# Performance work log

Measured on AMD Instinct MI355X. Metric: run time of the kernel, lower is better.

## Reference

```python
import jax, jax.numpy as jnp
import numpy as np

N, E, IN, OUT, R = 50000, 800000, 256, 256, 8
BN_EPS = 1e-5


def setup_inputs() -> dict:
    key = jax.random.key(0)
    ks = jax.random.split(key, 8)
    x = jax.random.normal(ks[0], (N, IN), dtype=jnp.float32)
    edge_index = jax.random.randint(ks[1], (2, E), 0, N, dtype=jnp.int64)
    # edge_attr: 5 float columns; column 4 carries the relation id in [0, R)
    edge_attr = jax.random.randint(ks[2], (E, 5), 0, R).astype(jnp.float32)
    # RGCNConv params (PyG defaults: root_weight=True, bias=True, aggr='mean')
    W = jax.random.normal(ks[3], (R, IN, OUT), dtype=jnp.float32) / np.sqrt(IN)
    root = jax.random.normal(ks[4], (IN, OUT), dtype=jnp.float32) / np.sqrt(IN)
    bias = jnp.zeros((OUT,), dtype=jnp.float32)
    # BatchNorm1d affine params
    gamma = jnp.ones((OUT,), dtype=jnp.float32)
    beta = jnp.zeros((OUT,), dtype=jnp.float32)
    # PReLU single shared slope (torch default init 0.25)
    prelu_a = jnp.asarray(0.25, dtype=jnp.float32)
    return {"x": x, "edge_index": edge_index, "edge_attr": edge_attr,
            "W": W, "root": root, "bias": bias,
            "gamma": gamma, "beta": beta, "prelu_a": prelu_a}


def _rgcn_block(x, edge_index, edge_type, W, root, bias, gamma, beta, prelu_a):
    src, dst = edge_index[0], edge_index[1]
    # per-(relation, dst) mean aggregation via a single segment_sum
    seg = edge_type.astype(jnp.int32) * N + dst.astype(jnp.int32)  # [E]
    msg_sum = jax.ops.segment_sum(x[src], seg, num_segments=R * N)  # [R*N, IN]
    cnt = jax.ops.segment_sum(jnp.ones((E,), x.dtype), seg, num_segments=R * N)
    mean = msg_sum.reshape(R, N, IN) / jnp.maximum(cnt, 1.0).reshape(R, N, 1)
    # relation-specific linear transforms, summed over relations, plus root + bias
    h = jnp.einsum('rni,rio->no', mean, W) + x @ root + bias  # [N, OUT]
    # BatchNorm1d (training mode: batch statistics over nodes)
    mu = jnp.mean(h, axis=0)
    var = jnp.mean(jnp.square(h - mu), axis=0)
    h = (h - mu) * jax.lax.rsqrt(var + BN_EPS) * gamma + beta
    # PReLU (single shared slope); dropout is identity at inference
    h = jnp.where(h > 0, h, prelu_a * h)
    # residual (in_channels == out_channels -> Identity projection)
    return h + x


def reference(x, edge_index, edge_attr, W, root, bias, gamma, beta, prelu_a):
    edge_type = edge_attr[:, 4].astype(jnp.int32)
    return _rgcn_block(x, edge_index, edge_type, W, root, bias, gamma, beta, prelu_a)
```

## Files before the change

### kernel.cpp

```cpp
#include <hip/hip_runtime.h>
#include <cstdio>
#include <cstdint>


constexpr int kN  = 50000;
constexpr int kE  = 800000;
constexpr int kR  = 8;
constexpr int kC  = 256;
constexpr int kK  = 2304;
constexpr int kNB = 782;

typedef __attribute__((ext_vector_type(8))) short bf16x8;
typedef __attribute__((ext_vector_type(4))) float f32x4;
typedef __attribute__((ext_vector_type(2))) unsigned int u32x2;

__device__ __forceinline__ unsigned short f2bf(float f) {
  unsigned u = __builtin_bit_cast(unsigned, f);
  u = u + 0x7FFFu + ((u >> 16) & 1u);
  return (unsigned short)(u >> 16);
}
__device__ __forceinline__ float bf2f(unsigned short s) {
  unsigned u = ((unsigned)s) << 16;
  return __builtin_bit_cast(float, u);
}

__global__ void k_count(const int* __restrict__ ei, const float* __restrict__ ea,
                        int* __restrict__ cnt) {
  int e = blockIdx.x * blockDim.x + threadIdx.x;
  if (e >= kE) return;
  int dst = ei[kE + e];
  int rel = (int)ea[(size_t)e * 5 + 4];
  if ((unsigned)dst >= (unsigned)kN || (unsigned)rel >= (unsigned)kR) return;
  atomicAdd(&cnt[rel * kN + dst], 1);
}

__global__ void k_convert_x(const float* __restrict__ x, unsigned short* __restrict__ xbf) {
  int i = (blockIdx.x * blockDim.x + threadIdx.x) * 4;
  if (i >= kN * kC) return;
  float4 v = *(const float4*)(x + i);
  ushort4 o;
  o.x = f2bf(v.x); o.y = f2bf(v.y); o.z = f2bf(v.z); o.w = f2bf(v.w);
  *(ushort4*)(xbf + i) = o;
}

__global__ void k_convert_w(const float* __restrict__ W, const float* __restrict__ root,
                            unsigned short* __restrict__ wbfT) {
  int t = blockIdx.x * blockDim.x + threadIdx.x;
  if (t >= kC * kK) return;
  int c = t / kK, k = t - c * kK;
  float v;
  if (k < kR * kC) {
    int r = k >> 8, kk = k & 255;
    v = W[(size_t)r * kC * kC + (size_t)kk * kC + c];
  } else {
    v = root[(size_t)(k - kR * kC) * kC + c];
  }
  wbfT[(size_t)c * kK + k] = f2bf(v);
}

__global__ void k_grp(const int* __restrict__ cnt, int* __restrict__ cursor,
                      int* __restrict__ gst, int* __restrict__ cur) {
  int wid = (blockIdx.x * blockDim.x + threadIdx.x) >> 6;
  int lane = threadIdx.x & 63;
  if (wid >= kR * kNB) return;
  int r = wid / kNB, db = (wid - r * kNB) * 64;
  int d = db + lane;
  int c = (d < kN) ? cnt[r * kN + d] : 0;
  int incl = c;
#pragma unroll
  for (int s = 1; s < 64; s <<= 1) {
    int v = __shfl_up(incl, s);
    if (lane >= s) incl += v;
  }
  int wtot = __shfl(incl, 63);
  int base = 0;
  if (lane == 63) base = atomicAdd(cursor, wtot);
  base = __shfl(base, 63);
  if (d < kN) { int o = base + incl - c; gst[r * kN + d] = o; cur[r * kN + d] = o; }
}

__global__ void k_fill(const int* __restrict__ ei, const float* __restrict__ ea,
                       int* __restrict__ cur, unsigned short* __restrict__ ebuf) {
  int e = blockIdx.x * blockDim.x + threadIdx.x;
  if (e >= kE) return;
  int src = ei[e];
  int dst = ei[kE + e];
  int rel = (int)ea[(size_t)e * 5 + 4];
  if ((unsigned)dst >= (unsigned)kN || (unsigned)rel >= (unsigned)kR) return;
  int pos = atomicAdd(&cur[rel * kN + dst], 1);
  ebuf[pos] = (unsigned short)src;
}

__global__ __launch_bounds__(512) void k_fused(const unsigned short* __restrict__ xbf,
                                               const unsigned short* __restrict__ wbfT,
                                               const unsigned short* __restrict__ ebuf,
                                               const int* __restrict__ gst,
                                               const int* __restrict__ cnt,
                                               const float* __restrict__ bias,
                                               float* __restrict__ out,
                                               float* __restrict__ cs,
                                               float* __restrict__ csq) {
  __shared__ __align__(16) unsigned short Ms[64 * 256];
  const int tid = threadIdx.x, lane = tid & 63, wv = tid >> 6;
  const int d0 = blockIdx.x * 64;
  const int dbase = d0 + wv * 8;
  f32x4 acc[4][2] = {};

  auto ms_store = [&](int row, float s0, float s1, float s2, float s3) {
    unsigned lo = (unsigned)f2bf(s0) | ((unsigned)f2bf(s1) << 16);
    unsigned hi = (unsigned)f2bf(s2) | ((unsigned)f2bf(s3) << 16);
    unsigned byte = (unsigned)(row * 512) + (((unsigned)(lane * 8)) ^ ((unsigned)((row & 7) << 4)));
    *(u32x2*)((char*)Ms + byte) = u32x2{lo, hi};
  };

  for (int r = 0; r < 9; ++r) {
    if (r < kR) {
      int vc = kN - dbase; vc = vc < 0 ? 0 : (vc > 8 ? 8 : vc);
      int gidx = 0;
      if (vc > 0) {
        int gb = r * kN + dbase;
        int myst = 0, myen = 0;
        if (lane < vc) { myst = gst[gb + lane]; myen = myst + cnt[gb + lane]; }
        int runSt = __shfl(myst, 0);
        int runEn = __shfl(myen, vc - 1);
        int curSt = runSt;
        int curEn = __shfl(myen, 0);
        float s0 = 0.f, s1 = 0.f, s2 = 0.f, s3 = 0.f;
        for (int base = runSt; base < runEn; base += 64) {
          int p = base + lane;
          int srcl = (p < runEn) ? (int)ebuf[p] : 0;
          int nn = runEn - base; if (nn > 64) nn = 64;
          for (int q = 0; q < nn; q += 4) {
            int i0 = __shfl(srcl, q);
            int i1 = __shfl(srcl, (q + 1) & 63);
            int i2 = __shfl(srcl, (q + 2) & 63);
            int i3 = __shfl(srcl, (q + 3) & 63);
            ushort4 v0 = *(const ushort4*)(xbf + (size_t)i0 * kC + lane * 4);
            ushort4 v1 = *(const ushort4*)(xbf + (size_t)i1 * kC + lane * 4);
            ushort4 v2 = *(const ushort4*)(xbf + (size_t)i2 * kC + lane * 4);
            ushort4 v3 = *(const ushort4*)(xbf + (size_t)i3 * kC + lane * 4);
            ushort4 vv[4] = {v0, v1, v2, v3};
#pragma unroll
            for (int i = 0; i < 4; ++i) {
              if (q + i >= nn) break;
              int pe = base + q + i;
              while (pe >= curEn) {
                int c = curEn - curSt;
                float sc = c > 0 ? 1.f / (float)c : 0.f;
                ms_store(wv * 8 + gidx, s0 * sc, s1 * sc, s2 * sc, s3 * sc);
                s0 = s1 = s2 = s3 = 0.f;
                ++gidx;
                curSt = curEn;
                curEn = __shfl(myen, gidx < vc ? gidx : vc - 1);
              }
              s0 += bf2f(vv[i].x); s1 += bf2f(vv[i].y);
              s2 += bf2f(vv[i].z); s3 += bf2f(vv[i].w);
            }
          }
        }
        while (gidx < vc) {
          int c = curEn - curSt;
          float sc = c > 0 ? 1.f / (float)c : 0.f;
          ms_store(wv * 8 + gidx, s0 * sc, s1 * sc, s2 * sc, s3 * sc);
          s0 = s1 = s2 = s3 = 0.f;
          ++gidx;
          if (gidx < vc) { curSt = curEn; curEn = __shfl(myen, gidx); }
        }
      }
      for (int g = gidx < 0 ? 0 : (vc > 0 ? vc : 0); g < 8; ++g)
        ms_store(wv * 8 + g, 0.f, 0.f, 0.f, 0.f);
    } else {
      for (int g = 0; g < 8; ++g) {
        int d = dbase + g;
        unsigned lo = 0, hi = 0;
        if (d < kN) {
          ushort4 v = *(const ushort4*)(xbf + (size_t)d * kC + lane * 4);
          lo = (unsigned)v.x | ((unsigned)v.y << 16);
          hi = (unsigned)v.z | ((unsigned)v.w << 16);
        }
        int row = wv * 8 + g;
        unsigned byte = (unsigned)(row * 512) + (((unsigned)(lane * 8)) ^ ((unsigned)((row & 7) << 4)));
        *(u32x2*)((char*)Ms + byte) = u32x2{lo, hi};
      }
    }
    __syncthreads();

    const int rbase = r * 256;
#pragma unroll
    for (int kk = 0; kk < 256; kk += 32) {
      const int koff = kk + (lane >> 4) * 8;
      bf16x8 a[4], b[2];
#pragma unroll
      for (int i = 0; i < 4; ++i) {
        int row = i * 16 + (lane & 15);
        unsigned byte = (unsigned)(row * 512) + (((unsigned)(koff * 2)) ^ ((unsigned)((row & 7) << 4)));
        a[i] = *(const bf16x8*)((const char*)Ms + byte);
      }
#pragma unroll
      for (int j = 0; j < 2; ++j) {
        int col = wv * 32 + j * 16 + (lane & 15);
        b[j] = *(const bf16x8*)(wbfT + (size_t)col * kK + rbase + koff);
      }
#pragma unroll
      for (int i = 0; i < 4; ++i)
#pragma unroll
        for (int j = 0; j < 2; ++j)
          acc[i][j] = __builtin_amdgcn_mfma_f32_16x16x32_bf16(a[i], b[j], acc[i][j], 0, 0, 0);
    }
    __syncthreads();
  }

#pragma unroll
  for (int j = 0; j < 2; ++j) {
    int col = wv * 32 + j * 16 + (lane & 15);
    float bv = bias[col];
    float s = 0.f, ss = 0.f;
#pragma unroll
    for (int i = 0; i < 4; ++i) {
      int rb = d0 + i * 16 + (lane >> 4) * 4;
#pragma unroll
      for (int q = 0; q < 4; ++q) {
        float v = acc[i][j][q];
        s += v; ss += v * v;
        int row = rb + q;
        if (row < kN) out[(size_t)row * kC + col] = v + bv;
      }
    }
    s  += __shfl_xor(s, 16);  s  += __shfl_xor(s, 32);
    ss += __shfl_xor(ss, 16); ss += __shfl_xor(ss, 32);
    if (lane < 16) { atomicAdd(&cs[col], s); atomicAdd(&csq[col], ss); }
  }
}

__global__ void k_final(float* __restrict__ h, const float* __restrict__ x,
                        const float* __restrict__ cs, const float* __restrict__ csq,
                        const float* __restrict__ bias,
                        const float* __restrict__ gamma, const float* __restrict__ beta,
                        const float* __restrict__ prelu) {
  int idx = (blockIdx.x * blockDim.x + threadIdx.x) * 4;
  if (idx >= kN * kC) return;
  int col = idx & 255;
  const float inv_n = 1.0f / (float)kN;
  float a = prelu[0];
  float4 hv = *(float4*)(h + idx);
  float4 xv = *(const float4*)(x + idx);
  float hr[4] = {hv.x, hv.y, hv.z, hv.w};
  float xr[4] = {xv.x, xv.y, xv.z, xv.w};
#pragma unroll
  for (int j = 0; j < 4; ++j) {
    int c = col + j;
    float mu_raw = cs[c] * inv_n;
    float var = csq[c] * inv_n - mu_raw * mu_raw;
    float mu  = mu_raw + bias[c];
    float k   = gamma[c] * rsqrtf(var + 1e-5f);
    float v   = (hr[j] - mu) * k + beta[c];
    v = v > 0.f ? v : a * v;
    hr[j] = v + xr[j];
  }
  *(float4*)(h + idx) = make_float4(hr[0], hr[1], hr[2], hr[3]);
}

extern "C" void kernel_launch(void* const* d_in, const int* in_sizes, int n_in,
                              void* d_out, int out_size, void* d_ws, size_t ws_size,
                              hipStream_t stream) {
  const float* x     = (const float*)d_in[0];
  const int*   ei    = (const int*)d_in[1];
  const float* ea    = (const float*)d_in[2];
  const float* W     = (const float*)d_in[3];
  const float* root  = (const float*)d_in[4];
  const float* bias  = (const float*)d_in[5];
  const float* gamma = (const float*)d_in[6];
  const float* beta  = (const float*)d_in[7];
  const float* prelu = (const float*)d_in[8];
  float* out = (float*)d_out;
  char* ws = (char*)d_ws;

  size_t o = 0;
  auto alloc = [&](size_t sz) { size_t r = o; o += (sz + 255) & ~(size_t)255; return r; };
  size_t xbf_o  = alloc((size_t)kN * kC * 2);
  size_t wbf_o  = alloc((size_t)kC * kK * 2);
  size_t cnt_o  = alloc((size_t)kR * kN * 4);
  size_t cs_o   = alloc(256 * 4);
  size_t csq_o  = alloc(256 * 4);
  size_t csr_o  = alloc(256);
  size_t zend   = o;
  size_t gst_o  = alloc((size_t)kR * kN * 4);
  size_t cur_o  = alloc((size_t)kR * kN * 4);
  size_t eb_o   = alloc((size_t)kE * 2);
  if (o > ws_size) {
    fprintf(stderr, "[RGCN kernel] ws too small: need %zu have %zu\n", o, ws_size);
    return;
  }

  unsigned short* xbf  = (unsigned short*)(ws + xbf_o);
  unsigned short* wbfT = (unsigned short*)(ws + wbf_o);
  int*   cnt    = (int*)(ws + cnt_o);
  float* cs     = (float*)(ws + cs_o);
  float* csq    = (float*)(ws + csq_o);
  int*   cursor = (int*)(ws + csr_o);
  int*   gst    = (int*)(ws + gst_o);
  int*   cur    = (int*)(ws + cur_o);
  unsigned short* ebuf = (unsigned short*)(ws + eb_o);

  hipMemsetAsync(ws + cnt_o, 0, zend - cnt_o, stream);
  k_count<<<(kE + 255) / 256, 256, 0, stream>>>(ei, ea, cnt);
  k_convert_x<<<(kN * kC / 4) / 256, 256, 0, stream>>>(x, xbf);
  k_convert_w<<<(kC * kK + 255) / 256, 256, 0, stream>>>(W, root, wbfT);
  k_grp<<<(kR * kNB * 64 + 255) / 256, 256, 0, stream>>>(cnt, cursor, gst, cur);
  k_fill<<<(kE + 255) / 256, 256, 0, stream>>>(ei, ea, cur, ebuf);
  k_fused<<<kNB, 512, 0, stream>>>(xbf, wbfT, ebuf, gst, cnt, bias, out, cs, csq);
  k_final<<<(kN * kC / 4) / 256, 256, 0, stream>>>(out, x, cs, csq, bias, gamma, beta, prelu);
}
```

Baseline: 415.0 us.

## Warp-specialize fused RGCN kernel into gather producers and MFMA consumers with double buffering

Splits the 8 waves of each block into 4 producer waves that gather and average neighbor rows into a double-buffered LDS tile, and 4 consumer waves that run the MFMA GEMM over each relation slice. The goal is to overlap the latency-bound gather with matrix math instead of alternating between them. Each consumer wave now holds twice the accumulators (64 columns), which raises register pressure, and only half the waves gather, so gather throughput per block drops. Separately, k_count packs dst and relation into one word so k_fill reads less edge_attr data.

```diff
diff --git a/kernel.cpp b/kernel.cpp
--- a/kernel.cpp
+++ b/kernel.cpp
@@ -23,14 +23,24 @@
   unsigned u = ((unsigned)s) << 16;
   return __builtin_bit_cast(float, u);
 }
+__device__ __forceinline__ void ms_put(unsigned short* buf, int row, int lane,
+                                       unsigned lo, unsigned hi) {
+  unsigned byte = (unsigned)(row * 512) +
+                  (((unsigned)(lane * 8)) ^ ((unsigned)((row & 7) << 4)));
+  *(u32x2*)((char*)buf + byte) = u32x2{lo, hi};
+}
 
 __global__ void k_count(const int* __restrict__ ei, const float* __restrict__ ea,
-                        int* __restrict__ cnt) {
+                        int* __restrict__ cnt, unsigned* __restrict__ pdr) {
   int e = blockIdx.x * blockDim.x + threadIdx.x;
   if (e >= kE) return;
   int dst = ei[kE + e];
   int rel = (int)ea[(size_t)e * 5 + 4];
-  if ((unsigned)dst >= (unsigned)kN || (unsigned)rel >= (unsigned)kR) return;
+  if ((unsigned)dst >= (unsigned)kN || (unsigned)rel >= (unsigned)kR) {
+    pdr[e] = 0xFFFFFFFFu;
+    return;
+  }
+  pdr[e] = (unsigned)dst | ((unsigned)rel << 16);
   atomicAdd(&cnt[rel * kN + dst], 1);
 }
 
@@ -79,16 +89,15 @@
   if (d < kN) { int o = base + incl - c; gst[r * kN + d] = o; cur[r * kN + d] = o; }
 }
 
-__global__ void k_fill(const int* __restrict__ ei, const float* __restrict__ ea,
+__global__ void k_fill(const int* __restrict__ ei, const unsigned* __restrict__ pdr,
                        int* __restrict__ cur, unsigned short* __restrict__ ebuf) {
   int e = blockIdx.x * blockDim.x + threadIdx.x;
   if (e >= kE) return;
-  int src = ei[e];
-  int dst = ei[kE + e];
-  int rel = (int)ea[(size_t)e * 5 + 4];
-  if ((unsigned)dst >= (unsigned)kN || (unsigned)rel >= (unsigned)kR) return;
+  unsigned pd = pdr[e];
+  if (pd == 0xFFFFFFFFu) return;
+  int dst = pd & 0xFFFF, rel = pd >> 16;
   int pos = atomicAdd(&cur[rel * kN + dst], 1);
-  ebuf[pos] = (unsigned short)src;
+  ebuf[pos] = (unsigned short)ei[e];
 }
 
 __global__ __launch_bounds__(512) void k_fused(const unsigned short* __restrict__ xbf,
@@ -100,135 +109,137 @@
                                                float* __restrict__ out,
                                                float* __restrict__ cs,
                                                float* __restrict__ csq) {
-  __shared__ __align__(16) unsigned short Ms[64 * 256];
+  __shared__ __align__(16) unsigned short Ms[2][64 * 256];
   const int tid = threadIdx.x, lane = tid & 63, wv = tid >> 6;
   const int d0 = blockIdx.x * 64;
-  const int dbase = d0 + wv * 8;
-  f32x4 acc[4][2] = {};
-
-  auto ms_store = [&](int row, float s0, float s1, float s2, float s3) {
-    unsigned lo = (unsigned)f2bf(s0) | ((unsigned)f2bf(s1) << 16);
-    unsigned hi = (unsigned)f2bf(s2) | ((unsigned)f2bf(s3) << 16);
-    unsigned byte = (unsigned)(row * 512) + (((unsigned)(lane * 8)) ^ ((unsigned)((row & 7) << 4)));
-    *(u32x2*)((char*)Ms + byte) = u32x2{lo, hi};
-  };
-
-  for (int r = 0; r < 9; ++r) {
-    if (r < kR) {
-      int vc = kN - dbase; vc = vc < 0 ? 0 : (vc > 8 ? 8 : vc);
-      int gidx = 0;
-      if (vc > 0) {
-        int gb = r * kN + dbase;
-        int myst = 0, myen = 0;
-        if (lane < vc) { myst = gst[gb + lane]; myen = myst + cnt[gb + lane]; }
-        int runSt = __shfl(myst, 0);
-        int runEn = __shfl(myen, vc - 1);
-        int curSt = runSt;
-        int curEn = __shfl(myen, 0);
-        float s0 = 0.f, s1 = 0.f, s2 = 0.f, s3 = 0.f;
-        for (int base = runSt; base < runEn; base += 64) {
-          int p = base + lane;
-          int srcl = (p < runEn) ? (int)ebuf[p] : 0;
-          int nn = runEn - base; if (nn > 64) nn = 64;
-          for (int q = 0; q < nn; q += 4) {
-            int i0 = __shfl(srcl, q);
-            int i1 = __shfl(srcl, (q + 1) & 63);
-            int i2 = __shfl(srcl, (q + 2) & 63);
-            int i3 = __shfl(srcl, (q + 3) & 63);
-            ushort4 v0 = *(const ushort4*)(xbf + (size_t)i0 * kC + lane * 4);
-            ushort4 v1 = *(const ushort4*)(xbf + (size_t)i1 * kC + lane * 4);
-            ushort4 v2 = *(const ushort4*)(xbf + (size_t)i2 * kC + lane * 4);
-            ushort4 v3 = *(const ushort4*)(xbf + (size_t)i3 * kC + lane * 4);
-            ushort4 vv[4] = {v0, v1, v2, v3};
-#pragma unroll
-            for (int i = 0; i < 4; ++i) {
-              if (q + i >= nn) break;
-              int pe = base + q + i;
-              while (pe >= curEn) {
-                int c = curEn - curSt;
-                float sc = c > 0 ? 1.f / (float)c : 0.f;
-                ms_store(wv * 8 + gidx, s0 * sc, s1 * sc, s2 * sc, s3 * sc);
-                s0 = s1 = s2 = s3 = 0.f;
-                ++gidx;
-                curSt = curEn;
-                curEn = __shfl(myen, gidx < vc ? gidx : vc - 1);
+
+  if (wv >= 4) {
+    const int p = wv - 4;
+    const int dbase = d0 + p * 16;
+    for (int r = 0; r < 9; ++r) {
+      unsigned short* buf = Ms[r & 1];
+      if (r < kR) {
+        int vc = kN - dbase; vc = vc < 0 ? 0 : (vc > 16 ? 16 : vc);
+        int gidx = 0;
+        if (vc > 0) {
+          int gb = r * kN + dbase;
+          int myst = 0, myen = 0;
+          if (lane < vc) { myst = gst[gb + lane]; myen = myst + cnt[gb + lane]; }
+          int runSt = __shfl(myst, 0);
+          int runEn = __shfl(myen, vc - 1);
+          int curSt = runSt;
+          int curEn = __shfl(myen, 0);
+          float s0 = 0.f, s1 = 0.f, s2 = 0.f, s3 = 0.f;
+          for (int base = runSt; base < runEn; base += 64) {
+            int pq = base + lane;
+            int srcl = (pq < runEn) ? (int)ebuf[pq] : 0;
+            int nn = runEn - base; if (nn > 64) nn = 64;
+            for (int q = 0; q < nn; q += 4) {
+              int i0 = __shfl(srcl, q);
+              int i1 = __shfl(srcl, (q + 1) & 63);
+              int i2 = __shfl(srcl, (q + 2) & 63);
+              int i3 = __shfl(srcl, (q + 3) & 63);
+              ushort4 v0 = *(const ushort4*)(xbf + (size_t)i0 * kC + lane * 4);
+              ushort4 v1 = *(const ushort4*)(xbf + (size_t)i1 * kC + lane * 4);
+              ushort4 v2 = *(const ushort4*)(xbf + (size_t)i2 * kC + lane * 4);
+              ushort4 v3 = *(const ushort4*)(xbf + (size_t)i3 * kC + lane * 4);
+              ushort4 vv[4] = {v0, v1, v2, v3};
+#pragma unroll
+              for (int i = 0; i < 4; ++i) {
+                if (q + i >= nn) break;
+                int pe = base + q + i;
+                while (pe >= curEn) {
+                  int c = curEn - curSt;
+                  float sc = c > 0 ? 1.f / (float)c : 0.f;
+                  ms_put(buf, p * 16 + gidx, lane,
+                         (unsigned)f2bf(s0 * sc) | ((unsigned)f2bf(s1 * sc) << 16),
+                         (unsigned)f2bf(s2 * sc) | ((unsigned)f2bf(s3 * sc) << 16));
+                  s0 = s1 = s2 = s3 = 0.f;
+                  ++gidx;
+                  curSt = curEn;
+                  curEn = __shfl(myen, gidx < vc ? gidx : vc - 1);
+                }
+                s0 += bf2f(vv[i].x); s1 += bf2f(vv[i].y);
+                s2 += bf2f(vv[i].z); s3 += bf2f(vv[i].w);
               }
-              s0 += bf2f(vv[i].x); s1 += bf2f(vv[i].y);
-              s2 += bf2f(vv[i].z); s3 += bf2f(vv[i].w);
             }
           }
-        }
-        while (gidx < vc) {
-          int c = curEn - curSt;
-          float sc = c > 0 ? 1.f / (float)c : 0.f;
-          ms_store(wv * 8 + gidx, s0 * sc, s1 * sc, s2 * sc, s3 * sc);
-          s0 = s1 = s2 = s3 = 0.f;
-          ++gidx;
-          if (gidx < vc) { curSt = curEn; curEn = __shfl(myen, gidx); }
+          while (gidx < vc) {
+            int c = curEn - curSt;
+            float sc = c > 0 ? 1.f / (float)c : 0.f;
+            ms_put(buf, p * 16 + gidx, lane,
+                   (unsigned)f2bf(s0 * sc) | ((unsigned)f2bf(s1 * sc) << 16),
+                   (unsigned)f2bf(s2 * sc) | ((unsigned)f2bf(s3 * sc) << 16));
+            s0 = s1 = s2 = s3 = 0.f;
+            ++gidx;
+            if (gidx < vc) { curSt = curEn; curEn = __shfl(myen, gidx); }
+          }
+        }
+        for (int g = (vc > 0 ? vc : 0); g < 16; ++g)
+          ms_put(buf, p * 16 + g, lane, 0u, 0u);
+      } else {
+        for (int g = 0; g < 16; ++g) {
+          int d = dbase + g;
+          unsigned lo = 0, hi = 0;
+          if (d < kN) {
+            ushort4 v = *(const ushort4*)(xbf + (size_t)d * kC + lane * 4);
+            lo = (unsigned)v.x | ((unsigned)v.y << 16);
+            hi = (unsigned)v.z | ((unsigned)v.w << 16);
+          }
+          ms_put(buf, p * 16 + g, lane, lo, hi);
         }
       }
-      for (int g = gidx < 0 ? 0 : (vc > 0 ? vc : 0); g < 8; ++g)
-        ms_store(wv * 8 + g, 0.f, 0.f, 0.f, 0.f);
-    } else {
-      for (int g = 0; g < 8; ++g) {
-        int d = dbase + g;
-        unsigned lo = 0, hi = 0;
-        if (d < kN) {
-          ushort4 v = *(const ushort4*)(xbf + (size_t)d * kC + lane * 4);
-          lo = (unsigned)v.x | ((unsigned)v.y << 16);
-          hi = (unsigned)v.z | ((unsigned)v.w << 16);
-        }
-        int row = wv * 8 + g;
-        unsigned byte = (unsigned)(row * 512) + (((unsigned)(lane * 8)) ^ ((unsigned)((row & 7) << 4)));
-        *(u32x2*)((char*)Ms + byte) = u32x2{lo, hi};
+      __syncthreads();
+    }
+  } else {
+    f32x4 acc[4][4] = {};
+    for (int r = 0; r < 9; ++r) {
+      __syncthreads();
+      const unsigned short* buf = Ms[r & 1];
+      const int rbase = r * 256;
+#pragma unroll
+      for (int kk = 0; kk < 256; kk += 32) {
+        const int koff = kk + (lane >> 4) * 8;
+        bf16x8 a[4], b[4];
+#pragma unroll
+        for (int i = 0; i < 4; ++i) {
+          int row = i * 16 + (lane & 15);
+          unsigned byte = (unsigned)(row * 512) +
+                          (((unsigned)(koff * 2)) ^ ((unsigned)((row & 7) << 4)));
+          a[i] = *(const bf16x8*)((const char*)buf + byte);
+        }
+#pragma unroll
+        for (int j = 0; j < 4; ++j) {
+          int col = wv * 64 + j * 16 + (lane & 15);
+          b[j] = *(const bf16x8*)(wbfT + (size_t)col * kK + rbase + koff);
+        }
+#pragma unroll
+        for (int i = 0; i < 4; ++i)
+#pragma unroll
+          for (int j = 0; j < 4; ++j)
+            acc[i][j] = __builtin_amdgcn_mfma_f32_16x16x32_bf16(a[i], b[j], acc[i][j], 0, 0, 0);
       }
     }
-    __syncthreads();
-
-    const int rbase = r * 256;
-#pragma unroll
-    for (int kk = 0; kk < 256; kk += 32) {
-      const int koff = kk + (lane >> 4) * 8;
-      bf16x8 a[4], b[2];
+#pragma unroll
+    for (int j = 0; j < 4; ++j) {
+      int col = wv * 64 + j * 16 + (lane & 15);
+      float bv = bias[col];
+      float s = 0.f, ss = 0.f;
 #pragma unroll
       for (int i = 0; i < 4; ++i) {
-        int row = i * 16 + (lane & 15);
-        unsigned byte = (unsigned)(row * 512) + (((unsigned)(koff * 2)) ^ ((unsigned)((row & 7) << 4)));
-        a[i] = *(const bf16x8*)((const char*)Ms + byte);
+        int rb = d0 + i * 16 + (lane >> 4) * 4;
+#pragma unroll
+        for (int q = 0; q < 4; ++q) {
+          float v = acc[i][j][q];
+          s += v; ss += v * v;
+          int row = rb + q;
+          if (row < kN) out[(size_t)row * kC + col] = v + bv;
+        }
       }
-#pragma unroll
-      for (int j = 0; j < 2; ++j) {
-        int col = wv * 32 + j * 16 + (lane & 15);
-        b[j] = *(const bf16x8*)(wbfT + (size_t)col * kK + rbase + koff);
-      }
-#pragma unroll
-      for (int i = 0; i < 4; ++i)
-#pragma unroll
-        for (int j = 0; j < 2; ++j)
-          acc[i][j] = __builtin_amdgcn_mfma_f32_16x16x32_bf16(a[i], b[j], acc[i][j], 0, 0, 0);
+      s  += __shfl_xor(s, 16);  s  += __shfl_xor(s, 32);
+      ss += __shfl_xor(ss, 16); ss += __shfl_xor(ss, 32);
+      if (lane < 16) { atomicAdd(&cs[col], s); atomicAdd(&csq[col], ss); }
     }
-    __syncthreads();
-  }
-
-#pragma unroll
-  for (int j = 0; j < 2; ++j) {
-    int col = wv * 32 + j * 16 + (lane & 15);
-    float bv = bias[col];
-    float s = 0.f, ss = 0.f;
-#pragma unroll
-    for (int i = 0; i < 4; ++i) {
-      int rb = d0 + i * 16 + (lane >> 4) * 4;
-#pragma unroll
-      for (int q = 0; q < 4; ++q) {
-        float v = acc[i][j][q];
-        s += v; ss += v * v;
-        int row = rb + q;
-        if (row < kN) out[(size_t)row * kC + col] = v + bv;
-      }
-    }
-    s  += __shfl_xor(s, 16);  s  += __shfl_xor(s, 32);
-    ss += __shfl_xor(ss, 16); ss += __shfl_xor(ss, 32);
-    if (lane < 16) { atomicAdd(&cs[col], s); atomicAdd(&csq[col], ss); }
   }
 }
 
@@ -287,6 +298,7 @@
   size_t gst_o  = alloc((size_t)kR * kN * 4);
   size_t cur_o  = alloc((size_t)kR * kN * 4);
   size_t eb_o   = alloc((size_t)kE * 2);
+  size_t pdr_o  = alloc((size_t)kE * 4);
   if (o > ws_size) {
     fprintf(stderr, "[RGCN kernel] ws too small: need %zu have %zu\n", o, ws_size);
     return;
@@ -294,20 +306,21 @@
 
   unsigned short* xbf  = (unsigned short*)(ws + xbf_o);
   unsigned short* wbfT = (unsigned short*)(ws + wbf_o);
-  int*   cnt    = (int*)(ws + cnt_o);
-  float* cs     = (float*)(ws + cs_o);
-  float* csq    = (float*)(ws + csq_o);
-  int*   cursor = (int*)(ws + csr_o);
-  int*   gst    = (int*)(ws + gst_o);
-  int*   cur    = (int*)(ws + cur_o);
+  int*      cnt    = (int*)(ws + cnt_o);
+  float*    cs     = (float*)(ws + cs_o);
+  float*    csq    = (float*)(ws + csq_o);
+  int*      cursor = (int*)(ws + csr_o);
+  int*      gst    = (int*)(ws + gst_o);
+  int*      cur    = (int*)(ws + cur_o);
   unsigned short* ebuf = (unsigned short*)(ws + eb_o);
+  unsigned* pdr    = (unsigned*)(ws + pdr_o);
 
   hipMemsetAsync(ws + cnt_o, 0, zend - cnt_o, stream);
-  k_count<<<(kE + 255) / 256, 256, 0, stream>>>(ei, ea, cnt);
+  k_count<<<(kE + 255) / 256, 256, 0, stream>>>(ei, ea, cnt, pdr);
   k_convert_x<<<(kN * kC / 4) / 256, 256, 0, stream>>>(x, xbf);
   k_convert_w<<<(kC * kK + 255) / 256, 256, 0, stream>>>(W, root, wbfT);
   k_grp<<<(kR * kNB * 64 + 255) / 256, 256, 0, stream>>>(cnt, cursor, gst, cur);
-  k_fill<<<(kE + 255) / 256, 256, 0, stream>>>(ei, ea, cur, ebuf);
+  k_fill<<<(kE + 255) / 256, 256, 0, stream>>>(ei, pdr, cur, ebuf);
   k_fused<<<kNB, 512, 0, stream>>>(xbf, wbfT, ebuf, gst, cnt, bias, out, cs, csq);
   k_final<<<(kN * kC / 4) / 256, 256, 0, stream>>>(out, x, cs, csq, bias, gamma, beta, prelu);
 }
```

After: 426.0 us. 1.03x slower.
